# Kernel optimization log

Hardware: AMD Instinct MI355X
Metric: run time of the kernel (lower is better)

The kernel has to match this reference:

```python
import jax, jax.numpy as jnp
import numpy as np

B, S, D = 2, 2048, 1024
H = 16
HD = D // H  # 64
SCALE = 1.0 / np.sqrt(HD).astype(np.float32)


def setup_inputs() -> dict:
    key = jax.random.key(0)
    ks = jax.random.split(key, 5)
    std = 0.02
    return {
        "x": jax.random.normal(ks[0], (B, S, D), dtype=jnp.float32),
        "W_qkv": jax.random.normal(ks[1], (D, 3 * D), dtype=jnp.float32) * std,
        "b_qkv": jnp.zeros((3 * D,), dtype=jnp.float32),
        "W_proj": jax.random.normal(ks[2], (D, D), dtype=jnp.float32) * std,
        "b_proj": jnp.zeros((D,), dtype=jnp.float32),
    }


def reference(x, W_qkv, b_qkv, W_proj, b_proj):
    bsz, seq_len, _ = x.shape
    qkv = x @ W_qkv + b_qkv  # [B,S,3D]
    qkv = qkv.reshape(bsz, seq_len, 3, H, HD)
    qkv = jnp.transpose(qkv, (2, 0, 3, 1, 4))  # [3,B,H,S,HD]
    q, k, v = qkv[0], qkv[1], qkv[2]
    scores = jnp.einsum("bhqd,bhkd->bhqk", q, k) * SCALE  # [B,H,S,S]
    causal = jnp.tril(jnp.ones((seq_len, seq_len), dtype=bool))
    scores = jnp.where(causal[None, None], scores, -jnp.inf)
    weights = jax.nn.softmax(scores, axis=-1)
    attn = jnp.einsum("bhqk,bhkd->bhqd", weights, v)  # [B,H,S,HD]
    attn = jnp.transpose(attn, (0, 2, 1, 3)).reshape(bsz, seq_len, H * HD)
    return attn @ W_proj + b_proj
```

## Files before the change

kernel.cpp:

```cpp
#include <hip/hip_runtime.h>
#include <stdint.h>

#define NB 2
#define NS 2048
#define ND 1024
#define NH 16
#define NHD 64
#define SCALE_QL2 0.1803368801111244f

typedef __attribute__((ext_vector_type(8))) short bf16x8;
typedef __attribute__((ext_vector_type(4))) float f32x4;
typedef __attribute__((ext_vector_type(16))) float f32x16;
typedef __attribute__((ext_vector_type(8))) unsigned short u16x8;

__device__ __forceinline__ unsigned short f2bf(float f) {
  union { float f; unsigned u; } v; v.f = f;
  unsigned r = v.u + 0x7FFFu + ((v.u >> 16) & 1u);
  return (unsigned short)(r >> 16);
}

__device__ __forceinline__ float bf2f(unsigned short u) {
  union { unsigned u; float f; } v; v.u = ((unsigned)u) << 16;
  return v.f;
}

__device__ __forceinline__ float fexp2(float x) { return __builtin_amdgcn_exp2f(x); }

__device__ __forceinline__ unsigned cvtpk(float a, float b) {
  unsigned r;
  asm("v_cvt_pk_bf16_f32 %0, %1, %2" : "=v"(r) : "v"(a), "v"(b));
  return r;
}

__device__ __forceinline__ void plswap(unsigned& a, unsigned& b) {
  asm("v_permlane32_swap_b32 %0, %1" : "+v"(a), "+v"(b));
}

__device__ __forceinline__ void gload16(const void* g, void* l) {
  __builtin_amdgcn_global_load_lds(
      (const __attribute__((address_space(1))) unsigned int*)g,
      (__attribute__((address_space(3))) unsigned int*)l, 16, 0, 0);
}


__global__ void cvt_x(const float* __restrict__ in, unsigned short* __restrict__ out) {
  int i = blockIdx.x * 256 + threadIdx.x;
  const float4* p = (const float4*)in + (size_t)i * 2;
  float4 a = p[0], b = p[1];
  u16x8 o;
  o[0] = f2bf(a.x); o[1] = f2bf(a.y); o[2] = f2bf(a.z); o[3] = f2bf(a.w);
  o[4] = f2bf(b.x); o[5] = f2bf(b.y); o[6] = f2bf(b.z); o[7] = f2bf(b.w);
  *((u16x8*)out + i) = o;
}

__global__ void transpose_cvt(const float* __restrict__ W, unsigned short* __restrict__ WT,
                              int rows, int cols) {
  __shared__ float tile[32][33];
  int bc = blockIdx.x * 32;
  int br = blockIdx.y * 32;
  int tx = threadIdx.x & 31, ty = threadIdx.x >> 5;
#pragma unroll
  for (int i = 0; i < 4; ++i)
    tile[ty + i * 8][tx] = W[(size_t)(br + ty + i * 8) * cols + bc + tx];
  __syncthreads();
#pragma unroll
  for (int i = 0; i < 4; ++i)
    WT[(size_t)(bc + ty + i * 8) * rows + br + tx] = f2bf(tile[tx][ty + i * 8]);
}

template <int EPI>
__global__ __launch_bounds__(256, 2) void gemm_bt(
    const unsigned short* __restrict__ A, const unsigned short* __restrict__ Bt,
    const float* __restrict__ bias, int NT,
    unsigned short* __restrict__ Oq, unsigned short* __restrict__ Ok,
    unsigned short* __restrict__ Ov, float* __restrict__ Of) {
  __shared__ __align__(16) unsigned short lA[128 * 64];
  __shared__ __align__(16) unsigned short lB[128 * 64];

  int bid = blockIdx.x;
  int cpx = gridDim.x >> 3;
  int swz = (bid & 7) * cpx + (bid >> 3);
  int mt = swz / NT, nt = swz % NT;
  int m0 = mt * 128, n0 = nt * 128;

  int t = threadIdx.x, lane = t & 63, w = t >> 6;
  int wm = w >> 1, wn = w & 1;

  f32x4 acc[4][4] = {};

  const char* gA = (const char*)(A + (size_t)m0 * 1024);
  const char* gB = (const char*)(Bt + (size_t)n0 * 1024);

  for (int kt = 0; kt < 16; ++kt) {
    __syncthreads();
#pragma unroll
    for (int r = 0; r < 4; ++r) {
      int L = r * 4096 + w * 1024 + lane * 16;
      int row = L >> 7, cb = L & 127;
      int scb = cb ^ ((row & 7) << 4);
      gload16(gA + (size_t)row * 2048 + kt * 128 + scb, (char*)lA + (L - lane * 16));
      gload16(gB + (size_t)row * 2048 + kt * 128 + scb, (char*)lB + (L - lane * 16));
    }
    __syncthreads();
#pragma unroll
    for (int kk = 0; kk < 2; ++kk) {
      bf16x8 af[4], bg[4];
#pragma unroll
      for (int mi = 0; mi < 4; ++mi) {
        int row = wm * 64 + mi * 16 + (lane & 15);
        int byte = row * 128 + ((kk * 64 + (lane >> 4) * 16) ^ ((row & 7) << 4));
        af[mi] = *(const bf16x8*)((const char*)lA + byte);
      }
#pragma unroll
      for (int ni = 0; ni < 4; ++ni) {
        int row = wn * 64 + ni * 16 + (lane & 15);
        int byte = row * 128 + ((kk * 64 + (lane >> 4) * 16) ^ ((row & 7) << 4));
        bg[ni] = *(const bf16x8*)((const char*)lB + byte);
      }
#pragma unroll
      for (int mi = 0; mi < 4; ++mi)
#pragma unroll
        for (int ni = 0; ni < 4; ++ni)
          acc[mi][ni] = __builtin_amdgcn_mfma_f32_16x16x32_bf16(af[mi], bg[ni], acc[mi][ni], 0, 0, 0);
    }
  }

#pragma unroll
  for (int mi = 0; mi < 4; ++mi)
#pragma unroll
    for (int ni = 0; ni < 4; ++ni) {
      int col = n0 + wn * 64 + ni * 16 + (lane & 15);
      float bv = bias[col];
#pragma unroll
      for (int r = 0; r < 4; ++r) {
        int row = m0 + wm * 64 + mi * 16 + (lane >> 4) * 4 + r;
        float v = acc[mi][ni][r] + bv;
        if (EPI == 0) {
          int which = col >> 10, dd = col & 1023;
          int h = dd >> 6, hd = dd & 63;
          int b = row >> 11, s = row & 2047;
          size_t bh = (size_t)(b * 16 + h);
          if (which == 0)      Oq[(bh * 2048 + s) * 64 + hd] = f2bf(v * SCALE_QL2);
          else if (which == 1) Ok[(bh * 2048 + s) * 64 + hd] = f2bf(v);
          else                 Ov[(bh * 64 + hd) * 2048 + s] = f2bf(v);
        } else {
          Of[(size_t)row * 1024 + col] = v;
        }
      }
    }
}

__global__ __launch_bounds__(256, 4) void attn_split(
    const unsigned short* __restrict__ Qb, const unsigned short* __restrict__ Kb,
    const unsigned short* __restrict__ Vt,
    unsigned short* __restrict__ PO, float* __restrict__ PML) {
  __shared__ __align__(16) unsigned short lK[2][64 * 64];
  __shared__ __align__(16) unsigned short lV[2][64 * 64];

  int id = blockIdx.x;
  int bh = id & 31;
  int slot = 39 - (id >> 5);
  int a, g;
  if (slot < 4)       { a = 0; g = slot; }
  else if (slot < 12) { a = 1; g = slot - 4; }
  else if (slot < 24) { a = 2; g = slot - 12; }
  else                { a = 3; g = slot - 24; }
  int Tg = (a == 0) ? g : (a == 1) ? (g >> 1) : (a == 2) ? ((g * 11) >> 5) : (g >> 2);
  int T  = a * 4 + Tg;
  int c  = g - Tg * (a + 1);
  int t0 = c * 8;
  int tend = min(t0 + 7, 2 * T + 1);

  int t = threadIdx.x, lane = t & 63, w = t >> 6;
  int lo = lane & 31, hi = lane >> 5;
  int q0w = T * 128 + w * 32;
  int itmaxw = 2 * T + (w >> 1);
  int swzb = (lo & 7) << 4;

  const unsigned short* Qg = Qb + ((size_t)bh * 2048 + q0w + lo) * 64 + hi * 8;
  bf16x8 qf[4];
#pragma unroll
  for (int kk = 0; kk < 4; ++kk) qf[kk] = *(const bf16x8*)(Qg + kk * 16);

  f32x16 o0 = {}, o1 = {};
  float m = -1e30f, lsum = 0.f;

  const char* Kg = (const char*)(Kb + (size_t)bh * 2048 * 64);
  const char* Vg = (const char*)(Vt + (size_t)bh * 64 * 2048);

  int Lb = t * 16;
  auto STAGE = [&](int buf, int tile) {
    int s0 = tile * 64;
#pragma unroll
    for (int r = 0; r < 2; ++r) {
      int L = r * 4096 + Lb;
      int row = L >> 7, cb = L & 127;
      int scb = cb ^ ((row & 7) << 4);
      gload16(Kg + (size_t)(s0 + row) * 128 + scb, (char*)&lK[buf][0] + (L - lane * 16));
      gload16(Vg + (size_t)row * 4096 + (size_t)s0 * 2 + scb, (char*)&lV[buf][0] + (L - lane * 16));
    }
  };

  STAGE(0, t0);

  int cur = 0;
  for (int it = t0; it <= tend; ++it) {
    if (it < tend) {
      STAGE(cur ^ 1, it + 1);
      asm volatile("s_waitcnt vmcnt(4)" ::: "memory");
    } else {
      asm volatile("s_waitcnt vmcnt(0)" ::: "memory");
    }
    asm volatile("s_barrier" ::: "memory");

    if (it <= itmaxw) {
      const char* bK = (const char*)&lK[cur][0];
      const char* bV = (const char*)&lV[cur][0];

      f32x16 sv0 = {}, sv1 = {};
      __builtin_amdgcn_s_setprio(1);
#pragma unroll
      for (int kk = 0; kk < 4; ++kk) {
        int dby = 32 * kk + 16 * hi;
        bf16x8 k0 = *(const bf16x8*)(bK + lo * 128 + (dby ^ swzb));
        bf16x8 k1 = *(const bf16x8*)(bK + (32 + lo) * 128 + (dby ^ swzb));
        sv0 = __builtin_amdgcn_mfma_f32_32x32x16_bf16(k0, qf[kk], sv0, 0, 0, 0);
        sv1 = __builtin_amdgcn_mfma_f32_32x32x16_bf16(k1, qf[kk], sv1, 0, 0, 0);
      }
      __builtin_amdgcn_s_setprio(0);

      if (it == itmaxw) {
        int qg2 = q0w + lo, s0 = it * 64;
#pragma unroll
        for (int r = 0; r < 16; ++r) {
          int kv = s0 + (r & 3) + 8 * (r >> 2) + 4 * hi;
          if (kv > qg2) sv0[r] = -1e30f;
          if (kv + 32 > qg2) sv1[r] = -1e30f;
        }
      }

      float rmax = -1e30f;
#pragma unroll
      for (int r = 0; r < 16; ++r) rmax = fmaxf(rmax, fmaxf(sv0[r], sv1[r]));
      rmax = fmaxf(rmax, __shfl_xor(rmax, 32));

      if (__any(rmax > m + 8.0f)) {
        float mn = fmaxf(m, rmax);
        float sf = fexp2(m - mn);
        m = mn; lsum *= sf;
#pragma unroll
        for (int r = 0; r < 16; ++r) {
          float s = __shfl(sf, (r & 3) + 8 * (r >> 2) + 4 * hi);
          o0[r] *= s; o1[r] *= s;
        }
      }

      float rsum = 0.f;
#pragma unroll
      for (int r = 0; r < 16; ++r) {
        sv0[r] = fexp2(sv0[r] - m); rsum += sv0[r];
        sv1[r] = fexp2(sv1[r] - m); rsum += sv1[r];
      }
      rsum += __shfl_xor(rsum, 32);
      lsum += rsum;

      bf16x8 pa[4];
#pragma unroll
      for (int h2 = 0; h2 < 2; ++h2) {
        const f32x16& P = h2 ? sv1 : sv0;
#pragma unroll
        for (int kp = 0; kp < 2; ++kp) {
          unsigned a0 = cvtpk(P[8 * kp + 0], P[8 * kp + 1]);
          unsigned a1 = cvtpk(P[8 * kp + 2], P[8 * kp + 3]);
          unsigned b0 = cvtpk(P[8 * kp + 4], P[8 * kp + 5]);
          unsigned b1 = cvtpk(P[8 * kp + 6], P[8 * kp + 7]);
          plswap(a0, b0); plswap(a1, b1);
          union { unsigned u[4]; bf16x8 v; } uu;
          uu.u[0] = a0; uu.u[1] = a1; uu.u[2] = b0; uu.u[3] = b1;
          pa[2 * h2 + kp] = uu.v;
        }
      }

      __builtin_amdgcn_s_setprio(1);
#pragma unroll
      for (int dh = 0; dh < 2; ++dh) {
        f32x16& oc = dh ? o1 : o0;
#pragma unroll
        for (int ks = 0; ks < 4; ++ks) {
          int kvby = 32 * ks + 16 * hi;
          bf16x8 vf = *(const bf16x8*)(bV + (32 * dh + lo) * 128 + (kvby ^ swzb));
          oc = __builtin_amdgcn_mfma_f32_32x32x16_bf16(pa[ks], vf, oc, 0, 0, 0);
        }
      }
      __builtin_amdgcn_s_setprio(0);
    }

    asm volatile("s_barrier" ::: "memory");
    cur ^= 1;
  }

  size_t pobase = (size_t)(bh * 40 + slot) * 128;
#pragma unroll
  for (int r = 0; r < 16; ++r) {
    int crow = (r & 3) + 8 * (r >> 2) + 4 * hi;
    size_t rowoff = (pobase + w * 32 + crow) * 64 + lo;
    PO[rowoff]      = f2bf(o0[r]);
    PO[rowoff + 32] = f2bf(o1[r]);
  }
  if (hi == 0) {
    size_t mlbase = (size_t)(bh * 40 + slot) * 256 + w * 32 + lo;
    PML[mlbase]       = m;
    PML[mlbase + 128] = lsum;
  }
}

__global__ void attn_combine(const unsigned short* __restrict__ PO,
                             const float* __restrict__ PML,
                             unsigned short* __restrict__ attn) {
  int id = blockIdx.x * 256 + threadIdx.x;
  int dg = id & 7;
  int s  = (id >> 3) & 2047;
  int bh = id >> 14;
  int T = s >> 7, a = T >> 2;
  int nc = a + 1;
  int slot0 = (a + 1) * (T - 2 * a);
  int r128 = s & 127;
  int pb = bh * 40 + slot0;

  float mv[4], lv[4];
#pragma unroll
  for (int c = 0; c < 4; ++c) {
    if (c < nc) {
      mv[c] = PML[(size_t)(pb + c) * 256 + r128];
      lv[c] = PML[(size_t)(pb + c) * 256 + 128 + r128];
    } else { mv[c] = -1e30f; lv[c] = 0.f; }
  }
  float M = fmaxf(fmaxf(mv[0], mv[1]), fmaxf(mv[2], mv[3]));
  float wv[4], L = 0.f;
#pragma unroll
  for (int c = 0; c < 4; ++c) { wv[c] = fexp2(mv[c] - M); L += wv[c] * lv[c]; }
  float rcpL = 1.0f / L;

  float acc[8] = {};
#pragma unroll
  for (int c = 0; c < 4; ++c) {
    if (c < nc) {
      bf16x8 p = *(const bf16x8*)(PO + ((size_t)(pb + c) * 128 + r128) * 64 + dg * 8);
#pragma unroll
      for (int j = 0; j < 8; ++j) acc[j] += wv[c] * bf2f((unsigned short)p[j]);
    }
  }
  u16x8 o;
#pragma unroll
  for (int j = 0; j < 8; ++j) o[j] = f2bf(acc[j] * rcpL);
  int b = bh >> 4, h = bh & 15;
  *(u16x8*)(attn + ((size_t)(b * 2048 + s)) * 1024 + h * 64 + dg * 8) = o;
}

extern "C" void kernel_launch(void* const* d_in, const int* in_sizes, int n_in,
                              void* d_out, int out_size, void* d_ws, size_t ws_size,
                              hipStream_t stream) {
  const float* x      = (const float*)d_in[0];
  const float* W_qkv  = (const float*)d_in[1];
  const float* b_qkv  = (const float*)d_in[2];
  const float* W_proj = (const float*)d_in[3];
  const float* b_proj = (const float*)d_in[4];
  float* out = (float*)d_out;

  char* ws = (char*)d_ws;
  const size_t MB = 1u << 20;
  unsigned short* xb     = (unsigned short*)(ws);
  unsigned short* WqkvT  = (unsigned short*)(ws + 8 * MB);
  unsigned short* WprojT = (unsigned short*)(ws + 14 * MB);
  unsigned short* Qb     = (unsigned short*)(ws + 16 * MB);
  unsigned short* Kb     = (unsigned short*)(ws + 24 * MB);
  unsigned short* Vt     = (unsigned short*)(ws + 32 * MB);
  unsigned short* PO     = (unsigned short*)(ws + 40 * MB);
  float*          PML    = (float*)(ws + 60 * MB);
  unsigned short* attn   = xb;

  cvt_x<<<2048, 256, 0, stream>>>(x, xb);
  transpose_cvt<<<dim3(96, 32), 256, 0, stream>>>(W_qkv, WqkvT, 1024, 3072);
  transpose_cvt<<<dim3(32, 32), 256, 0, stream>>>(W_proj, WprojT, 1024, 1024);
  gemm_bt<0><<<768, 256, 0, stream>>>(xb, WqkvT, b_qkv, 24, Qb, Kb, Vt, nullptr);
  attn_split<<<1280, 256, 0, stream>>>(Qb, Kb, Vt, PO, PML);
  attn_combine<<<2048, 256, 0, stream>>>(PO, PML, attn);
  gemm_bt<1><<<256, 256, 0, stream>>>(attn, WprojT, b_proj, 8, nullptr, nullptr, nullptr, out);
}
```

Baseline: 124.6 us.

## Use 256x256 double-buffered tiles for the QKV projection GEMM

Replaces the 128x128 QKV GEMM with a new kernel that uses 256x256 tiles, 512 threads and double-buffered LDS, prefetching the next K tile while MFMAs run on the current one. The larger tile raises arithmetic intensity and cuts global loads per FLOP. The overlap hides load latency. In exchange, the grid drops to 192 blocks at one block per CU, so the 256-CU device is not fully occupied, and LDS use reaches 128KB per block. The output-projection GEMM loses its template epilogue but is otherwise unchanged.

```diff
diff --git a/kernel.cpp b/kernel.cpp
--- a/kernel.cpp
+++ b/kernel.cpp
@@ -68,12 +68,105 @@
     WT[(size_t)(bc + ty + i * 8) * rows + br + tx] = f2bf(tile[tx][ty + i * 8]);
 }
 
-template <int EPI>
+__global__ __launch_bounds__(512, 1) void gemm256(
+    const unsigned short* __restrict__ A, const unsigned short* __restrict__ Bt,
+    const float* __restrict__ bias,
+    unsigned short* __restrict__ Oq, unsigned short* __restrict__ Ok,
+    unsigned short* __restrict__ Ov) {
+  __shared__ __align__(16) unsigned short lA[2][256 * 64];
+  __shared__ __align__(16) unsigned short lB[2][256 * 64];
+
+  int bid = blockIdx.x;
+  int cpx = gridDim.x >> 3;
+  int swz = (bid & 7) * cpx + (bid >> 3);
+  int mt = swz / 12, nt = swz % 12;
+  int m0 = mt * 256, n0 = nt * 256;
+
+  int t = threadIdx.x, lane = t & 63, w = t >> 6;
+  int wm = w >> 2, wn = w & 3;
+
+  f32x4 acc[8][4] = {};
+
+  const char* gA = (const char*)(A + (size_t)m0 * 1024);
+  const char* gB = (const char*)(Bt + (size_t)n0 * 1024);
+
+  auto SCHUNK = [&](int buf, int kt, int c) {
+    int L = c * 8192 + t * 16;
+    int row = L >> 7, cb = L & 127;
+    int scb = cb ^ ((row & 7) << 4);
+    gload16(gA + (size_t)row * 2048 + kt * 128 + scb, (char*)&lA[buf][0] + (L - lane * 16));
+    gload16(gB + (size_t)row * 2048 + kt * 128 + scb, (char*)&lB[buf][0] + (L - lane * 16));
+  };
+
+#pragma unroll
+  for (int c = 0; c < 4; ++c) SCHUNK(0, 0, c);
+
+  int cur = 0;
+  for (int kt = 0; kt < 16; ++kt) {
+    bf16x8 af[8];
+#pragma unroll
+    for (int p = 0; p < 4; ++p) {
+      int kk = p >> 1, nh = p & 1;
+      if (kt + 1 < 16) SCHUNK(cur ^ 1, kt + 1, p);
+      if (p == 0) {
+        if (kt + 1 < 16) asm volatile("s_waitcnt vmcnt(2)" ::: "memory");
+        else             asm volatile("s_waitcnt vmcnt(0)" ::: "memory");
+        __builtin_amdgcn_s_barrier();
+      }
+      if (nh == 0) {
+#pragma unroll
+        for (int mi = 0; mi < 8; ++mi) {
+          int row = wm * 128 + mi * 16 + (lane & 15);
+          int byte = row * 128 + ((kk * 64 + (lane >> 4) * 16) ^ ((row & 7) << 4));
+          af[mi] = *(const bf16x8*)((const char*)&lA[cur][0] + byte);
+        }
+      }
+      bf16x8 bg[2];
+#pragma unroll
+      for (int nj = 0; nj < 2; ++nj) {
+        int row = wn * 64 + (nh * 2 + nj) * 16 + (lane & 15);
+        int byte = row * 128 + ((kk * 64 + (lane >> 4) * 16) ^ ((row & 7) << 4));
+        bg[nj] = *(const bf16x8*)((const char*)&lB[cur][0] + byte);
+      }
+      asm volatile("s_waitcnt lgkmcnt(0)" ::: "memory");
+      __builtin_amdgcn_sched_barrier(0);
+      __builtin_amdgcn_s_setprio(1);
+#pragma unroll
+      for (int mi = 0; mi < 8; ++mi)
+#pragma unroll
+        for (int nj = 0; nj < 2; ++nj)
+          acc[mi][nh * 2 + nj] =
+              __builtin_amdgcn_mfma_f32_16x16x32_bf16(af[mi], bg[nj], acc[mi][nh * 2 + nj], 0, 0, 0);
+      __builtin_amdgcn_s_setprio(0);
+      __builtin_amdgcn_s_barrier();
+    }
+    cur ^= 1;
+  }
+
+#pragma unroll
+  for (int mi = 0; mi < 8; ++mi)
+#pragma unroll
+    for (int ni = 0; ni < 4; ++ni) {
+      int col = n0 + wn * 64 + ni * 16 + (lane & 15);
+      float bv = bias[col];
+#pragma unroll
+      for (int r = 0; r < 4; ++r) {
+        int row = m0 + wm * 128 + mi * 16 + (lane >> 4) * 4 + r;
+        float v = acc[mi][ni][r] + bv;
+        int which = col >> 10, dd = col & 1023;
+        int h = dd >> 6, hd = dd & 63;
+        int b = row >> 11, s = row & 2047;
+        size_t bh = (size_t)(b * 16 + h);
+        if (which == 0)      Oq[(bh * 2048 + s) * 64 + hd] = f2bf(v * SCALE_QL2);
+        else if (which == 1) Ok[(bh * 2048 + s) * 64 + hd] = f2bf(v);
+        else                 Ov[(bh * 64 + hd) * 2048 + s] = f2bf(v);
+      }
+    }
+}
+
 __global__ __launch_bounds__(256, 2) void gemm_bt(
     const unsigned short* __restrict__ A, const unsigned short* __restrict__ Bt,
-    const float* __restrict__ bias, int NT,
-    unsigned short* __restrict__ Oq, unsigned short* __restrict__ Ok,
-    unsigned short* __restrict__ Ov, float* __restrict__ Of) {
+    const float* __restrict__ bias, int NT, float* __restrict__ Of) {
   __shared__ __align__(16) unsigned short lA[128 * 64];
   __shared__ __align__(16) unsigned short lB[128 * 64];
 
@@ -134,18 +227,7 @@
 #pragma unroll
       for (int r = 0; r < 4; ++r) {
         int row = m0 + wm * 64 + mi * 16 + (lane >> 4) * 4 + r;
-        float v = acc[mi][ni][r] + bv;
-        if (EPI == 0) {
-          int which = col >> 10, dd = col & 1023;
-          int h = dd >> 6, hd = dd & 63;
-          int b = row >> 11, s = row & 2047;
-          size_t bh = (size_t)(b * 16 + h);
-          if (which == 0)      Oq[(bh * 2048 + s) * 64 + hd] = f2bf(v * SCALE_QL2);
-          else if (which == 1) Ok[(bh * 2048 + s) * 64 + hd] = f2bf(v);
-          else                 Ov[(bh * 64 + hd) * 2048 + s] = f2bf(v);
-        } else {
-          Of[(size_t)row * 1024 + col] = v;
-        }
+        Of[(size_t)row * 1024 + col] = acc[mi][ni][r] + bv;
       }
     }
 }
@@ -382,8 +464,8 @@
   cvt_x<<<2048, 256, 0, stream>>>(x, xb);
   transpose_cvt<<<dim3(96, 32), 256, 0, stream>>>(W_qkv, WqkvT, 1024, 3072);
   transpose_cvt<<<dim3(32, 32), 256, 0, stream>>>(W_proj, WprojT, 1024, 1024);
-  gemm_bt<0><<<768, 256, 0, stream>>>(xb, WqkvT, b_qkv, 24, Qb, Kb, Vt, nullptr);
+  gemm256<<<192, 512, 0, stream>>>(xb, WqkvT, b_qkv, Qb, Kb, Vt);
   attn_split<<<1280, 256, 0, stream>>>(Qb, Kb, Vt, PO, PML);
   attn_combine<<<2048, 256, 0, stream>>>(PO, PML, attn);
-  gemm_bt<1><<<256, 256, 0, stream>>>(attn, WprojT, b_proj, 8, nullptr, nullptr, nullptr, out);
-}
+  gemm_bt<<<256, 256, 0, stream>>>(attn, WprojT, b_proj, 8, out);
+}
```

Measured after the change: 154.3 us. 23.8% more time.
